# Kernel optimization log

Hardware: AMD Instinct MI355X
Metric: run time of the kernel (lower is better)

## Reference

```python
import jax, jax.numpy as jnp
import numpy as np

SCALE = 1.0 / np.sqrt(256.0)  # 1/sqrt(hidden_dim)


def setup_inputs() -> dict:
    key = jax.random.key(0)
    ks = jax.random.split(key, 9)
    N, C, H, W = 32, 256, 32, 32
    D, T = 256, 512
    s = lambda k, shape, fan: jax.random.normal(k, shape, jnp.float32) / np.sqrt(fan)
    return {
        "x": jax.random.normal(ks[0], (N, C, H, W), jnp.float32),
        "t": jax.random.normal(ks[1], (N, T), jnp.float32),
        "W_t": s(ks[2], (C, T), T),
        "b_t": jnp.zeros((C,), jnp.float32),
        "Wq": s(ks[3], (D, C), C),
        "Wk": s(ks[4], (D, C), C),
        "Wv": s(ks[5], (D, C), C),
        "Wp": s(ks[6], (C, D), D),
        "bp": jnp.zeros((C,), jnp.float32),
    }


def reference(x, t, W_t, b_t, Wq, Wk, Wv, Wp, bp):
    N, C, H, W = x.shape
    h = x
    # time embedding: Linear + ReLU, broadcast over spatial dims
    temb = jax.nn.relu(t @ W_t.T + b_t)  # [N, C]
    x = x + temb[:, :, None, None]
    # transpose(1,3): [N, C, H, W] -> [N, W, H, C]
    xc = jnp.transpose(x, (0, 3, 2, 1))
    q = xc @ Wq.T  # [N, W, H, D]
    k = xc @ Wk.T
    v = xc @ Wv.T
    # full spatial attention scores: [N, W, H, w, h]
    qk = jnp.einsum('NWHd,Nwhd->NWHwh', q, k) * SCALE
    qk = jax.nn.softmax(qk.reshape(N, W, H, W * H), axis=-1)
    qk = qk.reshape(N, W, H, W, H)
    out = jnp.einsum('NWHwh,Nwhd->NWHd', qk, v)  # [N, W, H, D]
    out = out @ Wp.T + bp  # [N, W, H, C]
    out = jnp.transpose(out, (0, 3, 2, 1))  # [N, C, H, W]
    return out + h
```

## Files before the change

kernel.cpp:

```cpp
#include <hip/hip_runtime.h>
#include <hip/hip_bf16.h>

#define NB 32
#define CD 256
#define SS 1024
#define DD 256
#define TT 512
#define QSCALE 0.09016844f

typedef __attribute__((ext_vector_type(8))) short s16x8;
typedef __attribute__((ext_vector_type(4))) short s16x4;
typedef __attribute__((ext_vector_type(4))) float f32x4;
typedef __attribute__((ext_vector_type(16))) float f32x16;
typedef __attribute__((ext_vector_type(4))) unsigned int u32x4;

__device__ __forceinline__ unsigned short f2bf(float f) {
  unsigned u = __builtin_bit_cast(unsigned, f);
  u = (u + 0x7FFFu + ((u >> 16) & 1u)) >> 16;
  return (unsigned short)u;
}
__device__ __forceinline__ float bf2f(unsigned short h) {
  return __builtin_bit_cast(float, ((unsigned)h) << 16);
}
__device__ __forceinline__ unsigned pk2(float a, float b) {
  float2 f2; f2.x = a; f2.y = b;
  __hip_bfloat162 h = __float22bfloat162_rn(f2);
  unsigned u;
  __builtin_memcpy(&u, &h, 4);
  return u;
}
__device__ __forceinline__ float asf(unsigned u) {
  return __builtin_bit_cast(float, u);
}
#define GLOAD16(gp, lp)                                                        \
  __builtin_amdgcn_global_load_lds(                                            \
      (const __attribute__((address_space(1))) unsigned int*)(const void*)(gp),\
      (__attribute__((address_space(3))) unsigned int*)(void*)(lp), 16, 0, 0)

__global__ __launch_bounds__(256) void k_misc(const float* __restrict__ t,
    const float* __restrict__ Wt, const float* __restrict__ bt, float* __restrict__ temb,
    const float* __restrict__ wq, const float* __restrict__ wk,
    const float* __restrict__ wv, const float* __restrict__ wp,
    unsigned short* __restrict__ dst) {
  const int b = blockIdx.x;
  if (b < 1024) {
    const int i = b * 256 + threadIdx.x;
    const int which = i >> 16, off = i & 65535;
    const float* s = which == 0 ? wq : which == 1 ? wk : which == 2 ? wv : wp;
    dst[i] = f2bf(s[off]);
  } else {
    const int n = b - 1024, c = threadIdx.x;
    const float4* tv = (const float4*)(t + (size_t)n * TT);
    const float4* wvv = (const float4*)(Wt + (size_t)c * TT);
    float acc = 0.f;
#pragma unroll 8
    for (int i = 0; i < TT / 4; ++i) {
      float4 a = tv[i], bb = wvv[i];
      acc += a.x * bb.x + a.y * bb.y + a.z * bb.z + a.w * bb.w;
    }
    acc += bt[c];
    temb[n * CD + c] = fmaxf(acc, 0.f);
  }
}

__global__ __launch_bounds__(256) void k_addT(const float* __restrict__ x,
    const float* __restrict__ temb, unsigned short* __restrict__ xb) {
  __shared__ float tile[32][33];
  const int tx = threadIdx.x & 31, ty = threadIdx.x >> 5;
  const int n = blockIdx.z, s0 = blockIdx.y * 32, c0 = blockIdx.x * 32;
#pragma unroll
  for (int i = 0; i < 4; ++i) {
    const int cc = ty + i * 8;
    tile[cc][tx] = x[((size_t)n * CD + c0 + cc) * SS + s0 + tx] + temb[n * CD + c0 + cc];
  }
  __syncthreads();
  unsigned short* op = xb + ((size_t)n * SS + s0) * CD + c0;
#pragma unroll
  for (int i = 0; i < 4; ++i) {
    const int ss = ty + i * 8;
    op[(size_t)ss * CD + tx] = f2bf(tile[tx][ss]);
  }
}

__global__ __launch_bounds__(256) void k_qkv(const unsigned short* __restrict__ A,
    const unsigned short* __restrict__ wb, unsigned short* __restrict__ qb,
    unsigned short* __restrict__ kb, unsigned short* __restrict__ vtb) {
  __shared__ __attribute__((aligned(16))) unsigned short As[128 * 32];
  __shared__ __attribute__((aligned(16))) unsigned short Bs[128 * 32];
  const int bid = blockIdx.x;
  const int xcd = bid & 7, idx = bid >> 3;
  const int n = xcd + 8 * (idx / 48);
  const int rem = idx % 48;
  const int which = rem >> 4, tt = rem & 15;
  const int s0 = (tt & 7) * 128;
  const int d0 = (tt >> 3) * 128;
  const unsigned short* B = wb + which * 65536;
  const int tid = threadIdx.x;
  const int lane = tid & 63, wid = tid >> 6;
  const int lo = lane & 15, hi = lane >> 4;
  const int wr = wid >> 1, wc = wid & 1;
  const unsigned short* An = A + (size_t)n * SS * CD;
  f32x4 acc[4][4] = {};
  for (int k0 = 0; k0 < CD; k0 += 32) {
#pragma unroll
    for (int i = 0; i < 2; ++i) {
      const int seg = i * 256 + wid * 64 + lane;
      const int row = seg >> 2, c8 = seg & 3;
      GLOAD16(An + (size_t)(s0 + row) * CD + k0 + c8 * 8, As + (size_t)(i * 256 + wid * 64) * 8);
      GLOAD16(B + (size_t)(d0 + row) * CD + k0 + c8 * 8, Bs + (size_t)(i * 256 + wid * 64) * 8);
    }
    __syncthreads();
    s16x8 a[4], b[4];
#pragma unroll
    for (int mi = 0; mi < 4; ++mi)
      a[mi] = *(const s16x8*)&As[(wr * 64 + mi * 16 + lo) * 32 + hi * 8];
#pragma unroll
    for (int ni = 0; ni < 4; ++ni)
      b[ni] = *(const s16x8*)&Bs[(wc * 64 + ni * 16 + lo) * 32 + hi * 8];
#pragma unroll
    for (int mi = 0; mi < 4; ++mi)
#pragma unroll
      for (int ni = 0; ni < 4; ++ni)
        acc[mi][ni] = __builtin_amdgcn_mfma_f32_16x16x32_bf16(a[mi], b[ni], acc[mi][ni], 0, 0, 0);
    __syncthreads();
  }
  if (which < 2) {
    const float osc = which == 0 ? QSCALE : 1.0f;
    unsigned short* On = (which == 0 ? qb : kb) + (size_t)n * SS * DD;
#pragma unroll
    for (int mi = 0; mi < 4; ++mi) {
      const int r0 = s0 + wr * 64 + mi * 16 + hi * 4;
#pragma unroll
      for (int ni = 0; ni < 4; ++ni) {
        const int col = d0 + wc * 64 + ni * 16 + lo;
#pragma unroll
        for (int r = 0; r < 4; ++r)
          On[(size_t)(r0 + r) * DD + col] = f2bf(acc[mi][ni][r] * osc);
      }
    }
  } else {
    unsigned short* On = vtb + (size_t)n * DD * SS;
#pragma unroll
    for (int mi = 0; mi < 4; ++mi) {
      const int r0 = s0 + wr * 64 + mi * 16 + hi * 4;
#pragma unroll
      for (int ni = 0; ni < 4; ++ni) {
        const int col = d0 + wc * 64 + ni * 16 + lo;
        s16x4 v;
#pragma unroll
        for (int r = 0; r < 4; ++r) v[r] = (short)f2bf(acc[mi][ni][r]);
        *(s16x4*)&On[(size_t)col * SS + r0] = v;
      }
    }
  }
}

__global__ __launch_bounds__(256, 2) void k_attn(const unsigned short* __restrict__ qb,
    const unsigned short* __restrict__ kb, const unsigned short* __restrict__ vtb,
    unsigned short* __restrict__ ob) {
  __shared__ __attribute__((aligned(16))) unsigned short lds[36864];
  const int bid = blockIdx.x;
  const int xcd = bid & 7, inner = bid >> 3;
  const int n = xcd + ((inner >> 4) << 3);
  const int sub = inner & 15;
  const int qt = sub & 7, dh = sub >> 3;
  const int tid = threadIdx.x, lane = tid & 63, w = tid >> 6;
  const int l31 = lane & 31, h = lane >> 5;
  const int dblk = dh * 128;
  const unsigned short* Kn = kb + (size_t)n * SS * DD;
  const unsigned short* Vn = vtb + ((size_t)n * DD + dblk) * SS;
  const int qrow = qt * 128 + w * 32 + l31;

  const unsigned short* Qp = qb + ((size_t)n * SS + qrow) * DD + h * 8;
  s16x8 qf[16];
#pragma unroll
  for (int ks = 0; ks < 16; ++ks) qf[ks] = *(const s16x8*)(Qp + ks * 16);

  f32x16 acc[4] = {};
  float lrun = 0.f;

  auto STAGE = [&](int buf, int jt) {
    const int j0 = jt * 32;
    unsigned short* KsB = lds + buf * 8192;
    unsigned short* VsB = lds + 24576 + buf * 4096;
#pragma unroll
    for (int i = 0; i < 4; ++i) {
      const int idx = i * 256 + w * 64 + lane;
      const int row = idx >> 5, c8 = idx & 31;
      GLOAD16(Kn + (size_t)(j0 + row) * DD + ((c8 ^ (row & 7)) << 3),
              KsB + (size_t)(i * 256 + w * 64) * 8);
    }
#pragma unroll
    for (int i = 0; i < 2; ++i) {
      const int idx = i * 256 + w * 64 + lane;
      const int row = idx >> 2, c8 = idx & 3;
      GLOAD16(Vn + (size_t)row * SS + j0 + ((c8 ^ ((row >> 1) & 3)) << 3),
              VsB + (size_t)(i * 256 + w * 64) * 8);
    }
  };

  STAGE(0, 0);
  STAGE(1, 1);
  __syncthreads();

  f32x16 scc = {};
#pragma unroll
  for (int ks = 0; ks < 16; ++ks) {
    const s16x8 kf = *(const s16x8*)&lds[l31 * 256 + ((((ks * 2 + h)) ^ (l31 & 7)) << 3)];
    scc = __builtin_amdgcn_mfma_f32_32x32x16_bf16(kf, qf[ks], scc, 0, 0, 0);
  }

  int sb = 2, qkb = 1, pvb = 0;
#pragma unroll 1
  for (int t = 0; t < 32; ++t) {
    if (t + 2 < 32) STAGE(sb, t + 2);
    f32x16 scn = {};
    if (t + 1 < 32) {
      const unsigned short* Ks = lds + qkb * 8192;
      __builtin_amdgcn_s_setprio(1);
#pragma unroll
      for (int ks = 0; ks < 16; ++ks) {
        const s16x8 kf = *(const s16x8*)&Ks[l31 * 256 + ((((ks * 2 + h)) ^ (l31 & 7)) << 3)];
        scn = __builtin_amdgcn_mfma_f32_32x32x16_bf16(kf, qf[ks], scn, 0, 0, 0);
      }
      __builtin_amdgcn_s_setprio(0);
    }
#pragma unroll
    for (int i = 0; i < 16; ++i) scc[i] = __builtin_amdgcn_exp2f(scc[i]);
    lrun += (((scc[0] + scc[1]) + (scc[2] + scc[3])) + ((scc[4] + scc[5]) + (scc[6] + scc[7]))) +
            (((scc[8] + scc[9]) + (scc[10] + scc[11])) + ((scc[12] + scc[13]) + (scc[14] + scc[15])));
    const unsigned wv0 = pk2(scc[0], scc[1]),   wv1 = pk2(scc[2], scc[3]);
    const unsigned wv2 = pk2(scc[4], scc[5]),   wv3 = pk2(scc[6], scc[7]);
    const unsigned wv4 = pk2(scc[8], scc[9]),   wv5 = pk2(scc[10], scc[11]);
    const unsigned wv6 = pk2(scc[12], scc[13]), wv7 = pk2(scc[14], scc[15]);
    auto r02 = __builtin_amdgcn_permlane32_swap(wv0, wv2, false, false);
    auto r13 = __builtin_amdgcn_permlane32_swap(wv1, wv3, false, false);
    auto r46 = __builtin_amdgcn_permlane32_swap(wv4, wv6, false, false);
    auto r57 = __builtin_amdgcn_permlane32_swap(wv5, wv7, false, false);
    const u32x4 pa0u = {r02[0], r13[0], r02[1], r13[1]};
    const u32x4 pa1u = {r46[0], r57[0], r46[1], r57[1]};
    const s16x8 pa0 = __builtin_bit_cast(s16x8, pa0u);
    const s16x8 pa1 = __builtin_bit_cast(s16x8, pa1u);
    const unsigned short* Vs = lds + 24576 + pvb * 4096;
    __builtin_amdgcn_s_setprio(1);
#pragma unroll
    for (int dc = 0; dc < 4; ++dc) {
      const s16x8 vf0 = *(const s16x8*)&Vs[(dc * 32 + l31) * 32 + ((h ^ ((l31 >> 1) & 3)) << 3)];
      acc[dc] = __builtin_amdgcn_mfma_f32_32x32x16_bf16(vf0, pa0, acc[dc], 0, 0, 0);
    }
#pragma unroll
    for (int dc = 0; dc < 4; ++dc) {
      const s16x8 vf1 = *(const s16x8*)&Vs[(dc * 32 + l31) * 32 + (((2 + h) ^ ((l31 >> 1) & 3)) << 3)];
      acc[dc] = __builtin_amdgcn_mfma_f32_32x32x16_bf16(vf1, pa1, acc[dc], 0, 0, 0);
    }
    __builtin_amdgcn_s_setprio(0);
    __syncthreads();
    scc = scn;
    sb = (sb + 1 == 3) ? 0 : sb + 1;
    qkb = (qkb + 1 == 3) ? 0 : qkb + 1;
    pvb = (pvb + 1 == 3) ? 0 : pvb + 1;
  }
  {
    auto rl = __builtin_amdgcn_permlane32_swap(__builtin_bit_cast(unsigned, lrun),
                                               __builtin_bit_cast(unsigned, lrun), false, false);
    lrun = asf(rl[0]) + asf(rl[1]);
  }
  const float inv = 1.0f / lrun;
  unsigned short* Op = ob + ((size_t)n * SS + qrow) * DD + dblk;
#pragma unroll
  for (int dc = 0; dc < 4; ++dc)
#pragma unroll
    for (int rg = 0; rg < 4; ++rg) {
      uint2 u;
      u.x = pk2(acc[dc][rg * 4 + 0] * inv, acc[dc][rg * 4 + 1] * inv);
      u.y = pk2(acc[dc][rg * 4 + 2] * inv, acc[dc][rg * 4 + 3] * inv);
      *(uint2*)(Op + dc * 32 + rg * 8 + h * 4) = u;
    }
}

__global__ __launch_bounds__(256) void k_proj(const unsigned short* __restrict__ ob,
    const unsigned short* __restrict__ wpb, const float* __restrict__ bp,
    const float* __restrict__ x, float* __restrict__ out) {
  __shared__ __attribute__((aligned(16))) unsigned short As[128 * 32];
  __shared__ __attribute__((aligned(16))) unsigned short Bs[128 * 32];
  const int bid = blockIdx.x;
  const int xcd = bid & 7, idx = bid >> 3;
  const int n = xcd + ((idx >> 4) << 3);
  const int rem = idx & 15;
  const int s0 = (rem & 7) * 128;
  const int c0 = (rem >> 3) * 128;
  const int tid = threadIdx.x;
  const int lane = tid & 63, wid = tid >> 6;
  const int lo = lane & 15, hi = lane >> 4;
  const int wr = wid >> 1, wc = wid & 1;
  const unsigned short* On = ob + (size_t)n * SS * DD;
  f32x4 acc[4][4] = {};
  for (int k0 = 0; k0 < DD; k0 += 32) {
#pragma unroll
    for (int i = 0; i < 2; ++i) {
      const int seg = i * 256 + wid * 64 + lane;
      const int row = seg >> 2, c8 = seg & 3;
      GLOAD16(wpb + (size_t)(c0 + row) * DD + k0 + c8 * 8, As + (size_t)(i * 256 + wid * 64) * 8);
      GLOAD16(On + (size_t)(s0 + row) * DD + k0 + c8 * 8, Bs + (size_t)(i * 256 + wid * 64) * 8);
    }
    __syncthreads();
    s16x8 a[4], b[4];
#pragma unroll
    for (int mi = 0; mi < 4; ++mi)
      a[mi] = *(const s16x8*)&As[(wr * 64 + mi * 16 + lo) * 32 + hi * 8];
#pragma unroll
    for (int ni = 0; ni < 4; ++ni)
      b[ni] = *(const s16x8*)&Bs[(wc * 64 + ni * 16 + lo) * 32 + hi * 8];
#pragma unroll
    for (int mi = 0; mi < 4; ++mi)
#pragma unroll
      for (int ni = 0; ni < 4; ++ni)
        acc[mi][ni] = __builtin_amdgcn_mfma_f32_16x16x32_bf16(a[mi], b[ni], acc[mi][ni], 0, 0, 0);
    __syncthreads();
  }
#pragma unroll
  for (int mi = 0; mi < 4; ++mi) {
#pragma unroll
    for (int r = 0; r < 4; ++r) {
      const int c = c0 + wr * 64 + mi * 16 + hi * 4 + r;
      const float bpc = bp[c];
      const size_t base = ((size_t)n * CD + c) * SS;
#pragma unroll
      for (int ni = 0; ni < 4; ++ni) {
        const int s = s0 + wc * 64 + ni * 16 + lo;
        out[base + s] = acc[mi][ni][r] + bpc + x[base + s];
      }
    }
  }
}

extern "C" void kernel_launch(void* const* d_in, const int* in_sizes, int n_in,
                              void* d_out, int out_size, void* d_ws, size_t ws_size,
                              hipStream_t stream) {
  const float* x  = (const float*)d_in[0];
  const float* t  = (const float*)d_in[1];
  const float* Wt = (const float*)d_in[2];
  const float* bt = (const float*)d_in[3];
  const float* Wq = (const float*)d_in[4];
  const float* Wk = (const float*)d_in[5];
  const float* Wv = (const float*)d_in[6];
  const float* Wp = (const float*)d_in[7];
  const float* bp = (const float*)d_in[8];
  char* ws = (char*)d_ws;
  float* temb        = (float*)ws;
  unsigned short* wb = (unsigned short*)(ws + 32768);
  unsigned short* xb = (unsigned short*)(ws + 557056);
  unsigned short* qb = (unsigned short*)(ws + 17334272);
  unsigned short* kb = (unsigned short*)(ws + 34111488);
  unsigned short* vtb = (unsigned short*)(ws + 50888704);
  unsigned short* ob = (unsigned short*)(ws + 67665920);
  float* out = (float*)d_out;

  k_misc<<<1056, 256, 0, stream>>>(t, Wt, bt, temb, Wq, Wk, Wv, Wp, wb);
  k_addT<<<dim3(8, 32, 32), 256, 0, stream>>>(x, temb, xb);
  k_qkv<<<1536, 256, 0, stream>>>(xb, wb, qb, kb, vtb);
  k_attn<<<512, 256, 0, stream>>>(qb, kb, vtb, ob);
  k_proj<<<512, 256, 0, stream>>>(ob, wb + 196608, bp, x, out);
}
```

Measured before the change: 136.1 us.

## Store Q and K in FP8 and compute attention scores with FP8 MFMA

The QKV kernel now writes Q and K as FP8, with the softmax scale split as a sqrt factor across both operands. The attention kernel loads them as 8-byte fragments and computes QK^T with the fp8 32x32x16 MFMA. This halves K staging bytes and shrinks LDS, which may allow more blocks per CU. The cost is lower score precision and a different swizzle layout.

Result: no change. 133.7 us (-1.8%).

```diff
diff --git a/kernel.cpp b/kernel.cpp
--- a/kernel.cpp
+++ b/kernel.cpp
@@ -6,7 +6,7 @@
 #define SS 1024
 #define DD 256
 #define TT 512
-#define QSCALE 0.09016844f
+#define OSC8 0.30028060f
 
 typedef __attribute__((ext_vector_type(8))) short s16x8;
 typedef __attribute__((ext_vector_type(4))) short s16x4;
@@ -31,6 +31,10 @@
 }
 __device__ __forceinline__ float asf(unsigned u) {
   return __builtin_bit_cast(float, u);
+}
+__device__ __forceinline__ unsigned char f2fp8(float v) {
+  int p = __builtin_amdgcn_cvt_pk_fp8_f32(v, v, 0, false);
+  return (unsigned char)(p & 0xFF);
 }
 #define GLOAD16(gp, lp)                                                        \
   __builtin_amdgcn_global_load_lds(                                            \
@@ -83,8 +87,8 @@
 }
 
 __global__ __launch_bounds__(256) void k_qkv(const unsigned short* __restrict__ A,
-    const unsigned short* __restrict__ wb, unsigned short* __restrict__ qb,
-    unsigned short* __restrict__ kb, unsigned short* __restrict__ vtb) {
+    const unsigned short* __restrict__ wb, unsigned char* __restrict__ qb8,
+    unsigned char* __restrict__ kb8, unsigned short* __restrict__ vtb) {
   __shared__ __attribute__((aligned(16))) unsigned short As[128 * 32];
   __shared__ __attribute__((aligned(16))) unsigned short Bs[128 * 32];
   const int bid = blockIdx.x;
@@ -125,8 +129,7 @@
     __syncthreads();
   }
   if (which < 2) {
-    const float osc = which == 0 ? QSCALE : 1.0f;
-    unsigned short* On = (which == 0 ? qb : kb) + (size_t)n * SS * DD;
+    unsigned char* On = (which == 0 ? qb8 : kb8) + (size_t)n * SS * DD;
 #pragma unroll
     for (int mi = 0; mi < 4; ++mi) {
       const int r0 = s0 + wr * 64 + mi * 16 + hi * 4;
@@ -135,7 +138,7 @@
         const int col = d0 + wc * 64 + ni * 16 + lo;
 #pragma unroll
         for (int r = 0; r < 4; ++r)
-          On[(size_t)(r0 + r) * DD + col] = f2bf(acc[mi][ni][r] * osc);
+          On[(size_t)(r0 + r) * DD + col] = f2fp8(acc[mi][ni][r] * OSC8);
       }
     }
   } else {
@@ -155,10 +158,10 @@
   }
 }
 
-__global__ __launch_bounds__(256, 2) void k_attn(const unsigned short* __restrict__ qb,
-    const unsigned short* __restrict__ kb, const unsigned short* __restrict__ vtb,
+__global__ __launch_bounds__(256, 2) void k_attn(const unsigned char* __restrict__ qb8,
+    const unsigned char* __restrict__ kb8, const unsigned short* __restrict__ vtb,
     unsigned short* __restrict__ ob) {
-  __shared__ __attribute__((aligned(16))) unsigned short lds[36864];
+  __shared__ __attribute__((aligned(16))) unsigned short lds[24576];
   const int bid = blockIdx.x;
   const int xcd = bid & 7, inner = bid >> 3;
   const int n = xcd + ((inner >> 4) << 3);
@@ -167,35 +170,35 @@
   const int tid = threadIdx.x, lane = tid & 63, w = tid >> 6;
   const int l31 = lane & 31, h = lane >> 5;
   const int dblk = dh * 128;
-  const unsigned short* Kn = kb + (size_t)n * SS * DD;
+  const unsigned char* Kn8 = kb8 + (size_t)n * SS * DD;
   const unsigned short* Vn = vtb + ((size_t)n * DD + dblk) * SS;
   const int qrow = qt * 128 + w * 32 + l31;
 
-  const unsigned short* Qp = qb + ((size_t)n * SS + qrow) * DD + h * 8;
-  s16x8 qf[16];
-#pragma unroll
-  for (int ks = 0; ks < 16; ++ks) qf[ks] = *(const s16x8*)(Qp + ks * 16);
+  const unsigned char* Qp8 = qb8 + ((size_t)n * SS + qrow) * DD + h * 8;
+  long qf8[16];
+#pragma unroll
+  for (int ks = 0; ks < 16; ++ks) qf8[ks] = *(const long*)(Qp8 + ks * 16);
 
   f32x16 acc[4] = {};
   float lrun = 0.f;
 
   auto STAGE = [&](int buf, int jt) {
     const int j0 = jt * 32;
-    unsigned short* KsB = lds + buf * 8192;
-    unsigned short* VsB = lds + 24576 + buf * 4096;
-#pragma unroll
-    for (int i = 0; i < 4; ++i) {
-      const int idx = i * 256 + w * 64 + lane;
-      const int row = idx >> 5, c8 = idx & 31;
-      GLOAD16(Kn + (size_t)(j0 + row) * DD + ((c8 ^ (row & 7)) << 3),
-              KsB + (size_t)(i * 256 + w * 64) * 8);
-    }
+    unsigned char* KsB = (unsigned char*)lds + buf * 8192;
+    unsigned char* VsB = (unsigned char*)lds + 24576 + buf * 8192;
 #pragma unroll
     for (int i = 0; i < 2; ++i) {
-      const int idx = i * 256 + w * 64 + lane;
-      const int row = idx >> 2, c8 = idx & 3;
+      const int id = i * 256 + w * 64 + lane;
+      const int row = id >> 4, p = id & 15;
+      GLOAD16(Kn8 + (size_t)(j0 + row) * DD + ((p ^ (row & 7)) << 4),
+              KsB + (size_t)(i * 256 + w * 64) * 16);
+    }
+#pragma unroll
+    for (int i = 0; i < 2; ++i) {
+      const int id = i * 256 + w * 64 + lane;
+      const int row = id >> 2, c8 = id & 3;
       GLOAD16(Vn + (size_t)row * SS + j0 + ((c8 ^ ((row >> 1) & 3)) << 3),
-              VsB + (size_t)(i * 256 + w * 64) * 8);
+              VsB + (size_t)(i * 256 + w * 64) * 16);
     }
   };
 
@@ -204,10 +207,13 @@
   __syncthreads();
 
   f32x16 scc = {};
-#pragma unroll
-  for (int ks = 0; ks < 16; ++ks) {
-    const s16x8 kf = *(const s16x8*)&lds[l31 * 256 + ((((ks * 2 + h)) ^ (l31 & 7)) << 3)];
-    scc = __builtin_amdgcn_mfma_f32_32x32x16_bf16(kf, qf[ks], scc, 0, 0, 0);
+  {
+    const unsigned char* Ks = (const unsigned char*)lds;
+#pragma unroll
+    for (int ks = 0; ks < 16; ++ks) {
+      const long kf = *(const long*)(Ks + l31 * 256 + ((ks ^ (l31 & 7)) << 4) + h * 8);
+      scc = __builtin_amdgcn_mfma_f32_32x32x16_fp8_fp8(kf, qf8[ks], scc, 0, 0, 0);
+    }
   }
 
   int sb = 2, qkb = 1, pvb = 0;
@@ -216,12 +222,12 @@
     if (t + 2 < 32) STAGE(sb, t + 2);
     f32x16 scn = {};
     if (t + 1 < 32) {
-      const unsigned short* Ks = lds + qkb * 8192;
+      const unsigned char* Ks = (const unsigned char*)lds + qkb * 8192;
       __builtin_amdgcn_s_setprio(1);
 #pragma unroll
       for (int ks = 0; ks < 16; ++ks) {
-        const s16x8 kf = *(const s16x8*)&Ks[l31 * 256 + ((((ks * 2 + h)) ^ (l31 & 7)) << 3)];
-        scn = __builtin_amdgcn_mfma_f32_32x32x16_bf16(kf, qf[ks], scn, 0, 0, 0);
+        const long kf = *(const long*)(Ks + l31 * 256 + ((ks ^ (l31 & 7)) << 4) + h * 8);
+        scn = __builtin_amdgcn_mfma_f32_32x32x16_fp8_fp8(kf, qf8[ks], scn, 0, 0, 0);
       }
       __builtin_amdgcn_s_setprio(0);
     }
@@ -241,7 +247,7 @@
     const u32x4 pa1u = {r46[0], r57[0], r46[1], r57[1]};
     const s16x8 pa0 = __builtin_bit_cast(s16x8, pa0u);
     const s16x8 pa1 = __builtin_bit_cast(s16x8, pa1u);
-    const unsigned short* Vs = lds + 24576 + pvb * 4096;
+    const unsigned short* Vs = (const unsigned short*)((const unsigned char*)lds + 24576 + pvb * 8192);
     __builtin_amdgcn_s_setprio(1);
 #pragma unroll
     for (int dc = 0; dc < 4; ++dc) {
@@ -350,15 +356,15 @@
   float* temb        = (float*)ws;
   unsigned short* wb = (unsigned short*)(ws + 32768);
   unsigned short* xb = (unsigned short*)(ws + 557056);
-  unsigned short* qb = (unsigned short*)(ws + 17334272);
-  unsigned short* kb = (unsigned short*)(ws + 34111488);
+  unsigned char* qb8 = (unsigned char*)(ws + 17334272);
+  unsigned char* kb8 = (unsigned char*)(ws + 34111488);
   unsigned short* vtb = (unsigned short*)(ws + 50888704);
   unsigned short* ob = (unsigned short*)(ws + 67665920);
   float* out = (float*)d_out;
 
   k_misc<<<1056, 256, 0, stream>>>(t, Wt, bt, temb, Wq, Wk, Wv, Wp, wb);
   k_addT<<<dim3(8, 32, 32), 256, 0, stream>>>(x, temb, xb);
-  k_qkv<<<1536, 256, 0, stream>>>(xb, wb, qb, kb, vtb);
-  k_attn<<<512, 256, 0, stream>>>(qb, kb, vtb, ob);
+  k_qkv<<<1536, 256, 0, stream>>>(xb, wb, qb8, kb8, vtb);
+  k_attn<<<512, 256, 0, stream>>>(qb8, kb8, vtb, ob);
   k_proj<<<512, 256, 0, stream>>>(ob, wb + 196608, bp, x, out);
 }
```
